# Optimization experiments

Measured on AMD Instinct MI355X. Metric: run time of the kernel, lower is better.

## Reference

```python
import jax, jax.numpy as jnp
import numpy as np

NODE_DIM = 128
EDGE_DIM = 16
HIDDEN = 128
B = 2
N = 20000
M = 320000


def setup_inputs() -> dict:
    key = jax.random.key(0)
    ks = jax.random.split(key, 20)

    def w(k, shape):
        return (jax.random.normal(k, shape, jnp.float32) / jnp.sqrt(shape[0])).astype(jnp.float32)

    X = jax.random.normal(ks[0], (B, N, NODE_DIM), jnp.float32)
    E = jax.random.normal(ks[1], (B, M, EDGE_DIM), jnp.float32)
    edges = jax.random.randint(ks[2], (B, M, 2), 0, N)
    return {
        "X": X, "E": E, "edges": edges,
        # node_mlp: Linear(node_dim,hidden) -> ReLU -> Linear(hidden,hidden)
        "nW1": w(ks[3], (NODE_DIM, HIDDEN)), "nb1": jnp.zeros((HIDDEN,), jnp.float32),
        "nW2": w(ks[4], (HIDDEN, HIDDEN)), "nb2": jnp.zeros((HIDDEN,), jnp.float32),
        # edge_mlp: Linear(2*node_dim+edge_dim,hidden) -> ReLU -> Linear(hidden,hidden)
        "eW1": w(ks[5], (2 * NODE_DIM + EDGE_DIM, HIDDEN)), "eb1": jnp.zeros((HIDDEN,), jnp.float32),
        "eW2": w(ks[6], (HIDDEN, HIDDEN)), "eb2": jnp.zeros((HIDDEN,), jnp.float32),
        # edge_proj: Linear(edge_dim, hidden)
        "pW": w(ks[7], (EDGE_DIM, HIDDEN)), "pb": jnp.zeros((HIDDEN,), jnp.float32),
        # read: Linear(2*hidden,64) -> ReLU -> Linear(64,2)
        "rW1": w(ks[8], (2 * HIDDEN, 64)), "rb1": jnp.zeros((64,), jnp.float32),
        "rW2": w(ks[9], (64, 2)), "rb2": jnp.zeros((2,), jnp.float32),
        "gate_scale": jnp.float32(2.0),
    }


def _forward_one(X, E, edges, nW1, nb1, nW2, nb2, eW1, eb1, eW2, eb2,
                 pW, pb, rW1, rb1, rW2, rb2, gate_scale):
    n_nodes = X.shape[0]
    n_edges = E.shape[0]
    # Hx = relu(node_mlp(X))  (node_mlp already ends without activation)
    Hx = jax.nn.relu(jax.nn.relu(X @ nW1 + nb1) @ nW2 + nb2)  # [N, H]
    # gate from 3rd edge-feature column (edge_dim >= 3)
    gate = jnp.clip(1.0 + gate_scale * E[:, 2:3], 0.0, 3.0)  # [M, 1]
    src = edges[:, 0]
    dst = edges[:, 1]
    # per-edge message: concat(X[i], X[j], E[k]) -> MLP -> relu -> * gate
    eij = jnp.concatenate([X[src], X[dst], E], axis=-1)  # [M, 2*node_dim+edge_dim]
    m = jax.nn.relu(jax.nn.relu(eij @ eW1 + eb1) @ eW2 + eb2) * gate  # [M, H]
    # scatter-add to both endpoints (sum order irrelevant)
    agg = (jax.ops.segment_sum(m, src, num_segments=n_nodes)
           + jax.ops.segment_sum(m, dst, num_segments=n_nodes))  # [N, H]
    # edge context: mean of gated edge projections
    edge_ctx = jnp.sum(gate * (E @ pW + pb), axis=0) / (n_edges + 1e-6)  # [H]
    H = Hx + agg
    feat = jnp.concatenate([H.mean(axis=0), edge_ctx], axis=0)  # [2H]
    return jax.nn.relu(feat @ rW1 + rb1) @ rW2 + rb2  # [2]


def reference(X, E, edges, nW1, nb1, nW2, nb2, eW1, eb1, eW2, eb2,
              pW, pb, rW1, rb1, rW2, rb2, gate_scale):
    fn = jax.vmap(_forward_one, in_axes=(0, 0, 0) + (None,) * 15)
    return fn(X, E, edges, nW1, nb1, nW2, nb2, eW1, eb1, eW2, eb2,
              pW, pb, rW1, rb1, rW2, rb2, gate_scale)  # [B, 2]
```

## Files before the change

### kernel.cpp

```cpp
#include <hip/hip_runtime.h>

typedef short bf16x8 __attribute__((ext_vector_type(8)));
typedef float f32x4 __attribute__((ext_vector_type(4)));

#define NB 2
#define NN 20000
#define ME 320000
#define STRIPES 64

__device__ __forceinline__ unsigned short f2bf(float f) {
  union { float f; unsigned int u; } v; v.f = f;
  unsigned int r = (v.u + 0x7FFFu + ((v.u >> 16) & 1u)) >> 16;
  return (unsigned short)r;
}

__device__ __forceinline__ f32x4 mfma16(bf16x8 a, bf16x8 b, f32x4 c) {
  return __builtin_amdgcn_mfma_f32_16x16x32_bf16(a, b, c, 0, 0, 0);
}


__global__ void cvt_x_kernel(const float* __restrict__ X, short* __restrict__ Xbf) {
  int i = blockIdx.x * 256 + threadIdx.x;
  const float4* p = reinterpret_cast<const float4*>(X) + (size_t)i * 2;
  float4 a = p[0], b = p[1];
  bf16x8 v;
  v[0]=(short)f2bf(a.x); v[1]=(short)f2bf(a.y); v[2]=(short)f2bf(a.z); v[3]=(short)f2bf(a.w);
  v[4]=(short)f2bf(b.x); v[5]=(short)f2bf(b.y); v[6]=(short)f2bf(b.z); v[7]=(short)f2bf(b.w);
  reinterpret_cast<bf16x8*>(Xbf)[i] = v;
}

__global__ void prep_w_kernel(const float* __restrict__ eW1, const float* __restrict__ eW2,
                              const float* __restrict__ nW1, const float* __restrict__ nW2,
                              const float* __restrict__ pW,
                              short* __restrict__ ew1T, short* __restrict__ ew2T,
                              short* __restrict__ nw1T, short* __restrict__ nw2T,
                              short* __restrict__ pwT) {
  int c = blockIdx.x;
  int t = threadIdx.x;
  for (int k = t; k < 288; k += 256)
    ew1T[c * 288 + k] = (k < 272) ? (short)f2bf(eW1[(size_t)k * 128 + c]) : (short)0;
  if (t < 128) {
    ew2T[c * 128 + t] = (short)f2bf(eW2[(size_t)t * 128 + c]);
    nw1T[c * 128 + t] = (short)f2bf(nW1[(size_t)t * 128 + c]);
    nw2T[c * 128 + t] = (short)f2bf(nW2[(size_t)t * 128 + c]);
  }
  if (t < 32) pwT[c * 32 + t] = (t < 16) ? (short)f2bf(pW[(size_t)t * 128 + c]) : (short)0;
}


template<bool XBF>
__global__ __launch_bounds__(256, 2) void edge_kernel(
    const short* __restrict__ Xbf, const float* __restrict__ X,
    const float* __restrict__ E, const int* __restrict__ edges,
    const short* __restrict__ ew1T, const short* __restrict__ ew2T,
    const short* __restrict__ pwT, const float* __restrict__ eb1,
    const float* __restrict__ eb2, const float* __restrict__ gsp,
    float* __restrict__ edge_acc) {
  __shared__ __align__(16) short A_lds[64 * 296];
  __shared__ __align__(16) short h1_lds[64 * 136];
  __shared__ float gate_lds[64];

  const int tid = threadIdx.x;
  const int lane = tid & 63;
  const int w = tid >> 6;
  const int fc = lane & 15;
  const int fg = lane >> 4;
  const int ncol0 = w * 32;
  const int b = blockIdx.y;

  const float gs = gsp[0];
  const float* E_b = E + (size_t)b * ME * 16;
  const int* edges_b = edges + (size_t)b * ME * 2;
  const short* Xbf_b = Xbf + (size_t)b * NN * 128;
  const float* X_b = X + (size_t)b * NN * 128;

  bf16x8 B1[2][9], B2[2][4], PWf[2];
  float eb1v[2], eb2v[2];
#pragma unroll
  for (int nt = 0; nt < 2; ++nt) {
    int col = ncol0 + nt * 16 + fc;
#pragma unroll
    for (int kt = 0; kt < 9; ++kt)
      B1[nt][kt] = *reinterpret_cast<const bf16x8*>(ew1T + col * 288 + kt * 32 + fg * 8);
#pragma unroll
    for (int kt = 0; kt < 4; ++kt)
      B2[nt][kt] = *reinterpret_cast<const bf16x8*>(ew2T + col * 128 + kt * 32 + fg * 8);
    PWf[nt] = *reinterpret_cast<const bf16x8*>(pwT + col * 32 + fg * 8);
    eb1v[nt] = eb1[col];
    eb2v[nt] = eb2[col];
  }

  float accm0 = 0.f, accm1 = 0.f, accp0 = 0.f, accp1 = 0.f, accg = 0.f;

  for (int it = 0; it < 4; ++it) {
    const int t = blockIdx.x * 4 + it;
    const int e0 = t * 64;
    if (XBF) {
#pragma unroll
      for (int p = 0; p < 8; ++p) {
        int row = p * 16 + (tid >> 4);
        int chunk = tid & 15;
        int e = row & 63, half = row >> 6;
        int node = edges_b[(size_t)(e0 + e) * 2 + half];
        uint4 v = reinterpret_cast<const uint4*>(Xbf_b + (size_t)node * 128)[chunk];
        *reinterpret_cast<uint4*>(&A_lds[e * 296 + half * 128 + chunk * 8]) = v;
      }
    } else {
#pragma unroll
      for (int p = 0; p < 16; ++p) {
        int slot = p * 256 + tid;
        int row = slot >> 5, chunk = slot & 31;
        int e = row & 63, half = row >> 6;
        int node = edges_b[(size_t)(e0 + e) * 2 + half];
        float4 f = reinterpret_cast<const float4*>(X_b + (size_t)node * 128)[chunk];
        ushort4 v; v.x = f2bf(f.x); v.y = f2bf(f.y); v.z = f2bf(f.z); v.w = f2bf(f.w);
        *reinterpret_cast<ushort4*>(&A_lds[e * 296 + half * 128 + chunk * 4]) = v;
      }
    }
    if (tid < 128) {
      int e = tid >> 1, half = tid & 1;
      const float4* pe = reinterpret_cast<const float4*>(E_b + (size_t)(e0 + e) * 16 + half * 8);
      float4 f0 = pe[0], f1 = pe[1];
      bf16x8 v;
      v[0]=(short)f2bf(f0.x); v[1]=(short)f2bf(f0.y); v[2]=(short)f2bf(f0.z); v[3]=(short)f2bf(f0.w);
      v[4]=(short)f2bf(f1.x); v[5]=(short)f2bf(f1.y); v[6]=(short)f2bf(f1.z); v[7]=(short)f2bf(f1.w);
      *reinterpret_cast<bf16x8*>(&A_lds[e * 296 + 256 + half * 8]) = v;
    } else {
      int e2 = (tid - 128) >> 1, half2 = (tid - 128) & 1;
      bf16x8 z = {0, 0, 0, 0, 0, 0, 0, 0};
      *reinterpret_cast<bf16x8*>(&A_lds[e2 * 296 + 272 + half2 * 8]) = z;
    }
    if (tid < 64) {
      float e2v = E_b[(size_t)(e0 + tid) * 16 + 2];
      gate_lds[tid] = fminf(fmaxf(1.f + gs * e2v, 0.f), 3.f);
    }
    __syncthreads();
    if (w == 0) accg += gate_lds[lane];

    f32x4 zf = {0.f, 0.f, 0.f, 0.f};
#pragma unroll
    for (int rt = 0; rt < 4; ++rt) {
      const short* arow = &A_lds[(rt * 16 + fc) * 296 + fg * 8];
      f32x4 a0 = zf, a1 = zf;
#pragma unroll
      for (int kt = 0; kt < 9; ++kt) {
        bf16x8 av = *reinterpret_cast<const bf16x8*>(arow + kt * 32);
        a0 = mfma16(av, B1[0][kt], a0);
        a1 = mfma16(av, B1[1][kt], a1);
      }
      bf16x8 av8 = *reinterpret_cast<const bf16x8*>(arow + 256);
      f32x4 p0 = mfma16(av8, PWf[0], zf);
      f32x4 p1 = mfma16(av8, PWf[1], zf);
#pragma unroll
      for (int r = 0; r < 4; ++r) {
        int row = rt * 16 + fg * 4 + r;
        float g = gate_lds[row];
        accp0 += p0[r] * g;
        accp1 += p1[r] * g;
        h1_lds[row * 136 + ncol0 + fc] = (short)f2bf(fmaxf(a0[r] + eb1v[0], 0.f));
        h1_lds[row * 136 + ncol0 + 16 + fc] = (short)f2bf(fmaxf(a1[r] + eb1v[1], 0.f));
      }
    }
    __syncthreads();
#pragma unroll
    for (int rt = 0; rt < 4; ++rt) {
      const short* hrow = &h1_lds[(rt * 16 + fc) * 136 + fg * 8];
      f32x4 a0 = zf, a1 = zf;
#pragma unroll
      for (int kt = 0; kt < 4; ++kt) {
        bf16x8 hv = *reinterpret_cast<const bf16x8*>(hrow + kt * 32);
        a0 = mfma16(hv, B2[0][kt], a0);
        a1 = mfma16(hv, B2[1][kt], a1);
      }
#pragma unroll
      for (int r = 0; r < 4; ++r) {
        int row = rt * 16 + fg * 4 + r;
        float g = gate_lds[row];
        accm0 += fmaxf(a0[r] + eb2v[0], 0.f) * g;
        accm1 += fmaxf(a1[r] + eb2v[1], 0.f) * g;
      }
    }
    __syncthreads();
  }

  accm0 += __shfl_xor(accm0, 16); accm0 += __shfl_xor(accm0, 32);
  accm1 += __shfl_xor(accm1, 16); accm1 += __shfl_xor(accm1, 32);
  accp0 += __shfl_xor(accp0, 16); accp0 += __shfl_xor(accp0, 32);
  accp1 += __shfl_xor(accp1, 16); accp1 += __shfl_xor(accp1, 32);
  const int stripe = blockIdx.x & (STRIPES - 1);
  float* base = edge_acc + ((size_t)b * STRIPES + stripe) * 264;
  if (fg == 0) {
    atomicAdd(base + ncol0 + fc, accm0);
    atomicAdd(base + ncol0 + 16 + fc, accm1);
    atomicAdd(base + 128 + ncol0 + fc, accp0);
    atomicAdd(base + 128 + ncol0 + 16 + fc, accp1);
  }
  if (w == 0) {
#pragma unroll
    for (int off = 1; off < 64; off <<= 1) accg += __shfl_xor(accg, off);
    if (lane == 0) atomicAdd(base + 256, accg);
  }
}


template<bool XBF>
__global__ __launch_bounds__(256, 2) void node_kernel(
    const short* __restrict__ Xbf, const float* __restrict__ X,
    const short* __restrict__ nw1T, const short* __restrict__ nw2T,
    const float* __restrict__ nb1, const float* __restrict__ nb2,
    float* __restrict__ node_acc) {
  __shared__ __align__(16) short A_lds[64 * 136];
  __shared__ __align__(16) short h1_lds[64 * 136];
  const int tid = threadIdx.x;
  const int lane = tid & 63;
  const int w = tid >> 6;
  const int fc = lane & 15;
  const int fg = lane >> 4;
  const int ncol0 = w * 32;
  const int b = blockIdx.y;
  const short* Xbf_b = Xbf + (size_t)b * NN * 128;
  const float* X_b = X + (size_t)b * NN * 128;

  bf16x8 B1[2][4], B2[2][4];
  float b1v[2], b2v[2];
#pragma unroll
  for (int nt = 0; nt < 2; ++nt) {
    int col = ncol0 + nt * 16 + fc;
#pragma unroll
    for (int kt = 0; kt < 4; ++kt) {
      B1[nt][kt] = *reinterpret_cast<const bf16x8*>(nw1T + col * 128 + kt * 32 + fg * 8);
      B2[nt][kt] = *reinterpret_cast<const bf16x8*>(nw2T + col * 128 + kt * 32 + fg * 8);
    }
    b1v[nt] = nb1[col];
    b2v[nt] = nb2[col];
  }
  float acc0 = 0.f, acc1 = 0.f;
  for (int t = blockIdx.x; t < 313; t += 157) {
    const int n0 = t * 64;
    if (XBF) {
#pragma unroll
      for (int p = 0; p < 4; ++p) {
        int row = p * 16 + (tid >> 4);
        int chunk = tid & 15;
        int node = n0 + row;
        uint4 v = {0, 0, 0, 0};
        if (node < NN) v = reinterpret_cast<const uint4*>(Xbf_b + (size_t)node * 128)[chunk];
        *reinterpret_cast<uint4*>(&A_lds[row * 136 + chunk * 8]) = v;
      }
    } else {
#pragma unroll
      for (int p = 0; p < 8; ++p) {
        int slot = p * 256 + tid;
        int row = slot >> 5, chunk = slot & 31;
        int node = n0 + row;
        ushort4 v = {0, 0, 0, 0};
        if (node < NN) {
          float4 f = reinterpret_cast<const float4*>(X_b + (size_t)node * 128)[chunk];
          v.x = f2bf(f.x); v.y = f2bf(f.y); v.z = f2bf(f.z); v.w = f2bf(f.w);
        }
        *reinterpret_cast<ushort4*>(&A_lds[row * 136 + chunk * 4]) = v;
      }
    }
    __syncthreads();
    f32x4 zf = {0.f, 0.f, 0.f, 0.f};
#pragma unroll
    for (int rt = 0; rt < 4; ++rt) {
      const short* arow = &A_lds[(rt * 16 + fc) * 136 + fg * 8];
      f32x4 a0 = zf, a1 = zf;
#pragma unroll
      for (int kt = 0; kt < 4; ++kt) {
        bf16x8 av = *reinterpret_cast<const bf16x8*>(arow + kt * 32);
        a0 = mfma16(av, B1[0][kt], a0);
        a1 = mfma16(av, B1[1][kt], a1);
      }
#pragma unroll
      for (int r = 0; r < 4; ++r) {
        int row = rt * 16 + fg * 4 + r;
        h1_lds[row * 136 + ncol0 + fc] = (short)f2bf(fmaxf(a0[r] + b1v[0], 0.f));
        h1_lds[row * 136 + ncol0 + 16 + fc] = (short)f2bf(fmaxf(a1[r] + b1v[1], 0.f));
      }
    }
    __syncthreads();
#pragma unroll
    for (int rt = 0; rt < 4; ++rt) {
      const short* hrow = &h1_lds[(rt * 16 + fc) * 136 + fg * 8];
      f32x4 a0 = zf, a1 = zf;
#pragma unroll
      for (int kt = 0; kt < 4; ++kt) {
        bf16x8 hv = *reinterpret_cast<const bf16x8*>(hrow + kt * 32);
        a0 = mfma16(hv, B2[0][kt], a0);
        a1 = mfma16(hv, B2[1][kt], a1);
      }
#pragma unroll
      for (int r = 0; r < 4; ++r) {
        int row = n0 + rt * 16 + fg * 4 + r;
        if (row < NN) {
          acc0 += fmaxf(a0[r] + b2v[0], 0.f);
          acc1 += fmaxf(a1[r] + b2v[1], 0.f);
        }
      }
    }
    __syncthreads();
  }
  acc0 += __shfl_xor(acc0, 16); acc0 += __shfl_xor(acc0, 32);
  acc1 += __shfl_xor(acc1, 16); acc1 += __shfl_xor(acc1, 32);
  if (fg == 0) {
    const int stripe = blockIdx.x & (STRIPES - 1);
    float* base = node_acc + ((size_t)b * STRIPES + stripe) * 128;
    atomicAdd(base + ncol0 + fc, acc0);
    atomicAdd(base + ncol0 + 16 + fc, acc1);
  }
}


__global__ void final_kernel(const float* __restrict__ edge_acc, const float* __restrict__ node_acc,
                             const float* __restrict__ pb, const float* __restrict__ rW1,
                             const float* __restrict__ rb1, const float* __restrict__ rW2,
                             const float* __restrict__ rb2, float* __restrict__ out) {
  int b = blockIdx.x;
  int j = threadIdx.x;
  __shared__ float feat[256];
  __shared__ float h[64];
  const float* ea = edge_acc + (size_t)b * STRIPES * 264;
  const float* na = node_acc + (size_t)b * STRIPES * 128;
  float ms = 0.f, ps = 0.f, hs = 0.f, gsum = 0.f;
  for (int s = 0; s < STRIPES; ++s) {
    ms += ea[s * 264 + j];
    ps += ea[s * 264 + 128 + j];
    hs += na[s * 128 + j];
    gsum += ea[s * 264 + 256];
  }
  feat[j] = (hs + 2.f * ms) * (1.f / (float)NN);
  feat[128 + j] = (ps + gsum * pb[j]) / ((float)ME + 1e-6f);
  __syncthreads();
  if (j < 64) {
    float a = rb1[j];
    for (int i = 0; i < 256; ++i) a += feat[i] * rW1[i * 64 + j];
    h[j] = fmaxf(a, 0.f);
  }
  __syncthreads();
  if (j < 2) {
    float a = rb2[j];
    for (int i = 0; i < 64; ++i) a += h[i] * rW2[i * 2 + j];
    out[b * 2 + j] = a;
  }
}


extern "C" void kernel_launch(void* const* d_in, const int* in_sizes, int n_in,
                              void* d_out, int out_size, void* d_ws, size_t ws_size,
                              hipStream_t stream) {
  const float* X = (const float*)d_in[0];
  const float* E = (const float*)d_in[1];
  const int* edges = (const int*)d_in[2];
  const float* nW1 = (const float*)d_in[3];
  const float* nb1 = (const float*)d_in[4];
  const float* nW2 = (const float*)d_in[5];
  const float* nb2 = (const float*)d_in[6];
  const float* eW1 = (const float*)d_in[7];
  const float* eb1 = (const float*)d_in[8];
  const float* eW2 = (const float*)d_in[9];
  const float* eb2 = (const float*)d_in[10];
  const float* pW = (const float*)d_in[11];
  const float* pb = (const float*)d_in[12];
  const float* rW1 = (const float*)d_in[13];
  const float* rb1 = (const float*)d_in[14];
  const float* rW2 = (const float*)d_in[15];
  const float* rb2 = (const float*)d_in[16];
  const float* gscale = (const float*)d_in[17];
  float* out = (float*)d_out;

  char* ws = (char*)d_ws;
  size_t off = 0;
  auto alloc = [&](size_t sz) -> void* {
    void* p = ws + off;
    off = (off + sz + 255) & ~(size_t)255;
    return p;
  };
  short* ew1T = (short*)alloc(288 * 128 * 2);
  short* ew2T = (short*)alloc(128 * 128 * 2);
  short* nw1T = (short*)alloc(128 * 128 * 2);
  short* nw2T = (short*)alloc(128 * 128 * 2);
  short* pwT  = (short*)alloc(32 * 128 * 2);
  size_t acc_floats = (size_t)NB * STRIPES * 264 + (size_t)NB * STRIPES * 128;
  float* acc = (float*)alloc(acc_floats * 4);
  float* edge_acc = acc;
  float* node_acc = acc + (size_t)NB * STRIPES * 264;
  size_t xbf_bytes = (size_t)NB * NN * 128 * 2;
  size_t off_before_xbf = off;
  short* Xbf = (short*)alloc(xbf_bytes);
  bool use_xbf = (off_before_xbf + xbf_bytes) <= ws_size;

  hipMemsetAsync(acc, 0, acc_floats * 4, stream);
  prep_w_kernel<<<dim3(128), dim3(256), 0, stream>>>(eW1, eW2, nW1, nW2, pW,
                                                     ew1T, ew2T, nw1T, nw2T, pwT);
  if (use_xbf) {
    cvt_x_kernel<<<dim3(2500), dim3(256), 0, stream>>>(X, Xbf);
    edge_kernel<true><<<dim3(1250, 2), dim3(256), 0, stream>>>(
        Xbf, X, E, edges, ew1T, ew2T, pwT, eb1, eb2, gscale, edge_acc);
    node_kernel<true><<<dim3(157, 2), dim3(256), 0, stream>>>(
        Xbf, X, nw1T, nw2T, nb1, nb2, node_acc);
  } else {
    edge_kernel<false><<<dim3(1250, 2), dim3(256), 0, stream>>>(
        Xbf, X, E, edges, ew1T, ew2T, pwT, eb1, eb2, gscale, edge_acc);
    node_kernel<false><<<dim3(157, 2), dim3(256), 0, stream>>>(
        Xbf, X, nw1T, nw2T, nb1, nb2, node_acc);
  }
  final_kernel<<<dim3(NB), dim3(128), 0, stream>>>(edge_acc, node_acc, pb, rW1, rb1, rW2, rb2, out);
}
```

Measured before the change: 242.1 us.

## Fuse X bf16 conversion into node kernel and software-pipeline edge gathers

Removes the separate X-to-bf16 conversion kernel: the node MLP kernel now converts X and writes the bf16 copy as it loads each tile, and runs first. The edge kernel becomes software-pipelined, with a double-buffered index and gate area, prefetching the next tile's gathered rows and edge features into registers while the current tile's MFMAs run. Each edge block now handles 8 tiles instead of 4, so fewer blocks reload the weight fragments. The cost is higher register pressure from holding prefetched data, which may hurt occupancy.

```diff
diff --git a/kernel.cpp b/kernel.cpp
--- a/kernel.cpp
+++ b/kernel.cpp
@@ -7,6 +7,7 @@
 #define NN 20000
 #define ME 320000
 #define STRIPES 64
+#define NT 8
 
 __device__ __forceinline__ unsigned short f2bf(float f) {
   union { float f; unsigned int u; } v; v.f = f;
@@ -14,19 +15,15 @@
   return (unsigned short)r;
 }
 
-__device__ __forceinline__ f32x4 mfma16(bf16x8 a, bf16x8 b, f32x4 c) {
-  return __builtin_amdgcn_mfma_f32_16x16x32_bf16(a, b, c, 0, 0, 0);
-}
-
-
-__global__ void cvt_x_kernel(const float* __restrict__ X, short* __restrict__ Xbf) {
-  int i = blockIdx.x * 256 + threadIdx.x;
-  const float4* p = reinterpret_cast<const float4*>(X) + (size_t)i * 2;
-  float4 a = p[0], b = p[1];
+__device__ __forceinline__ bf16x8 pack2(float4 a, float4 b) {
   bf16x8 v;
   v[0]=(short)f2bf(a.x); v[1]=(short)f2bf(a.y); v[2]=(short)f2bf(a.z); v[3]=(short)f2bf(a.w);
   v[4]=(short)f2bf(b.x); v[5]=(short)f2bf(b.y); v[6]=(short)f2bf(b.z); v[7]=(short)f2bf(b.w);
-  reinterpret_cast<bf16x8*>(Xbf)[i] = v;
+  return v;
+}
+
+__device__ __forceinline__ f32x4 mfma16(bf16x8 a, bf16x8 b, f32x4 c) {
+  return __builtin_amdgcn_mfma_f32_16x16x32_bf16(a, b, c, 0, 0, 0);
 }
 
 __global__ void prep_w_kernel(const float* __restrict__ eW1, const float* __restrict__ eW2,
@@ -48,164 +45,9 @@
 }
 
 
-template<bool XBF>
-__global__ __launch_bounds__(256, 2) void edge_kernel(
-    const short* __restrict__ Xbf, const float* __restrict__ X,
-    const float* __restrict__ E, const int* __restrict__ edges,
-    const short* __restrict__ ew1T, const short* __restrict__ ew2T,
-    const short* __restrict__ pwT, const float* __restrict__ eb1,
-    const float* __restrict__ eb2, const float* __restrict__ gsp,
-    float* __restrict__ edge_acc) {
-  __shared__ __align__(16) short A_lds[64 * 296];
-  __shared__ __align__(16) short h1_lds[64 * 136];
-  __shared__ float gate_lds[64];
-
-  const int tid = threadIdx.x;
-  const int lane = tid & 63;
-  const int w = tid >> 6;
-  const int fc = lane & 15;
-  const int fg = lane >> 4;
-  const int ncol0 = w * 32;
-  const int b = blockIdx.y;
-
-  const float gs = gsp[0];
-  const float* E_b = E + (size_t)b * ME * 16;
-  const int* edges_b = edges + (size_t)b * ME * 2;
-  const short* Xbf_b = Xbf + (size_t)b * NN * 128;
-  const float* X_b = X + (size_t)b * NN * 128;
-
-  bf16x8 B1[2][9], B2[2][4], PWf[2];
-  float eb1v[2], eb2v[2];
-#pragma unroll
-  for (int nt = 0; nt < 2; ++nt) {
-    int col = ncol0 + nt * 16 + fc;
-#pragma unroll
-    for (int kt = 0; kt < 9; ++kt)
-      B1[nt][kt] = *reinterpret_cast<const bf16x8*>(ew1T + col * 288 + kt * 32 + fg * 8);
-#pragma unroll
-    for (int kt = 0; kt < 4; ++kt)
-      B2[nt][kt] = *reinterpret_cast<const bf16x8*>(ew2T + col * 128 + kt * 32 + fg * 8);
-    PWf[nt] = *reinterpret_cast<const bf16x8*>(pwT + col * 32 + fg * 8);
-    eb1v[nt] = eb1[col];
-    eb2v[nt] = eb2[col];
-  }
-
-  float accm0 = 0.f, accm1 = 0.f, accp0 = 0.f, accp1 = 0.f, accg = 0.f;
-
-  for (int it = 0; it < 4; ++it) {
-    const int t = blockIdx.x * 4 + it;
-    const int e0 = t * 64;
-    if (XBF) {
-#pragma unroll
-      for (int p = 0; p < 8; ++p) {
-        int row = p * 16 + (tid >> 4);
-        int chunk = tid & 15;
-        int e = row & 63, half = row >> 6;
-        int node = edges_b[(size_t)(e0 + e) * 2 + half];
-        uint4 v = reinterpret_cast<const uint4*>(Xbf_b + (size_t)node * 128)[chunk];
-        *reinterpret_cast<uint4*>(&A_lds[e * 296 + half * 128 + chunk * 8]) = v;
-      }
-    } else {
-#pragma unroll
-      for (int p = 0; p < 16; ++p) {
-        int slot = p * 256 + tid;
-        int row = slot >> 5, chunk = slot & 31;
-        int e = row & 63, half = row >> 6;
-        int node = edges_b[(size_t)(e0 + e) * 2 + half];
-        float4 f = reinterpret_cast<const float4*>(X_b + (size_t)node * 128)[chunk];
-        ushort4 v; v.x = f2bf(f.x); v.y = f2bf(f.y); v.z = f2bf(f.z); v.w = f2bf(f.w);
-        *reinterpret_cast<ushort4*>(&A_lds[e * 296 + half * 128 + chunk * 4]) = v;
-      }
-    }
-    if (tid < 128) {
-      int e = tid >> 1, half = tid & 1;
-      const float4* pe = reinterpret_cast<const float4*>(E_b + (size_t)(e0 + e) * 16 + half * 8);
-      float4 f0 = pe[0], f1 = pe[1];
-      bf16x8 v;
-      v[0]=(short)f2bf(f0.x); v[1]=(short)f2bf(f0.y); v[2]=(short)f2bf(f0.z); v[3]=(short)f2bf(f0.w);
-      v[4]=(short)f2bf(f1.x); v[5]=(short)f2bf(f1.y); v[6]=(short)f2bf(f1.z); v[7]=(short)f2bf(f1.w);
-      *reinterpret_cast<bf16x8*>(&A_lds[e * 296 + 256 + half * 8]) = v;
-    } else {
-      int e2 = (tid - 128) >> 1, half2 = (tid - 128) & 1;
-      bf16x8 z = {0, 0, 0, 0, 0, 0, 0, 0};
-      *reinterpret_cast<bf16x8*>(&A_lds[e2 * 296 + 272 + half2 * 8]) = z;
-    }
-    if (tid < 64) {
-      float e2v = E_b[(size_t)(e0 + tid) * 16 + 2];
-      gate_lds[tid] = fminf(fmaxf(1.f + gs * e2v, 0.f), 3.f);
-    }
-    __syncthreads();
-    if (w == 0) accg += gate_lds[lane];
-
-    f32x4 zf = {0.f, 0.f, 0.f, 0.f};
-#pragma unroll
-    for (int rt = 0; rt < 4; ++rt) {
-      const short* arow = &A_lds[(rt * 16 + fc) * 296 + fg * 8];
-      f32x4 a0 = zf, a1 = zf;
-#pragma unroll
-      for (int kt = 0; kt < 9; ++kt) {
-        bf16x8 av = *reinterpret_cast<const bf16x8*>(arow + kt * 32);
-        a0 = mfma16(av, B1[0][kt], a0);
-        a1 = mfma16(av, B1[1][kt], a1);
-      }
-      bf16x8 av8 = *reinterpret_cast<const bf16x8*>(arow + 256);
-      f32x4 p0 = mfma16(av8, PWf[0], zf);
-      f32x4 p1 = mfma16(av8, PWf[1], zf);
-#pragma unroll
-      for (int r = 0; r < 4; ++r) {
-        int row = rt * 16 + fg * 4 + r;
-        float g = gate_lds[row];
-        accp0 += p0[r] * g;
-        accp1 += p1[r] * g;
-        h1_lds[row * 136 + ncol0 + fc] = (short)f2bf(fmaxf(a0[r] + eb1v[0], 0.f));
-        h1_lds[row * 136 + ncol0 + 16 + fc] = (short)f2bf(fmaxf(a1[r] + eb1v[1], 0.f));
-      }
-    }
-    __syncthreads();
-#pragma unroll
-    for (int rt = 0; rt < 4; ++rt) {
-      const short* hrow = &h1_lds[(rt * 16 + fc) * 136 + fg * 8];
-      f32x4 a0 = zf, a1 = zf;
-#pragma unroll
-      for (int kt = 0; kt < 4; ++kt) {
-        bf16x8 hv = *reinterpret_cast<const bf16x8*>(hrow + kt * 32);
-        a0 = mfma16(hv, B2[0][kt], a0);
-        a1 = mfma16(hv, B2[1][kt], a1);
-      }
-#pragma unroll
-      for (int r = 0; r < 4; ++r) {
-        int row = rt * 16 + fg * 4 + r;
-        float g = gate_lds[row];
-        accm0 += fmaxf(a0[r] + eb2v[0], 0.f) * g;
-        accm1 += fmaxf(a1[r] + eb2v[1], 0.f) * g;
-      }
-    }
-    __syncthreads();
-  }
-
-  accm0 += __shfl_xor(accm0, 16); accm0 += __shfl_xor(accm0, 32);
-  accm1 += __shfl_xor(accm1, 16); accm1 += __shfl_xor(accm1, 32);
-  accp0 += __shfl_xor(accp0, 16); accp0 += __shfl_xor(accp0, 32);
-  accp1 += __shfl_xor(accp1, 16); accp1 += __shfl_xor(accp1, 32);
-  const int stripe = blockIdx.x & (STRIPES - 1);
-  float* base = edge_acc + ((size_t)b * STRIPES + stripe) * 264;
-  if (fg == 0) {
-    atomicAdd(base + ncol0 + fc, accm0);
-    atomicAdd(base + ncol0 + 16 + fc, accm1);
-    atomicAdd(base + 128 + ncol0 + fc, accp0);
-    atomicAdd(base + 128 + ncol0 + 16 + fc, accp1);
-  }
-  if (w == 0) {
-#pragma unroll
-    for (int off = 1; off < 64; off <<= 1) accg += __shfl_xor(accg, off);
-    if (lane == 0) atomicAdd(base + 256, accg);
-  }
-}
-
-
-template<bool XBF>
+template<bool WRITEBF>
 __global__ __launch_bounds__(256, 2) void node_kernel(
-    const short* __restrict__ Xbf, const float* __restrict__ X,
+    const float* __restrict__ X, short* __restrict__ Xbf,
     const short* __restrict__ nw1T, const short* __restrict__ nw2T,
     const float* __restrict__ nb1, const float* __restrict__ nb2,
     float* __restrict__ node_acc) {
@@ -218,8 +60,8 @@
   const int fg = lane >> 4;
   const int ncol0 = w * 32;
   const int b = blockIdx.y;
-  const short* Xbf_b = Xbf + (size_t)b * NN * 128;
   const float* X_b = X + (size_t)b * NN * 128;
+  short* Xbf_b = Xbf + (size_t)b * NN * 128;
 
   bf16x8 B1[2][4], B2[2][4];
   float b1v[2], b2v[2];
@@ -234,73 +76,61 @@
     b1v[nt] = nb1[col];
     b2v[nt] = nb2[col];
   }
+
+  const int n0 = blockIdx.x * 64;
+#pragma unroll
+  for (int p = 0; p < 8; ++p) {
+    int slot = p * 256 + tid;
+    int row = slot >> 5, chunk = slot & 31;
+    int node = n0 + row;
+    ushort4 v = {0, 0, 0, 0};
+    if (node < NN) {
+      float4 f = *reinterpret_cast<const float4*>(X_b + (size_t)node * 128 + chunk * 4);
+      v.x = f2bf(f.x); v.y = f2bf(f.y); v.z = f2bf(f.z); v.w = f2bf(f.w);
+      if (WRITEBF) *reinterpret_cast<ushort4*>(Xbf_b + (size_t)node * 128 + chunk * 4) = v;
+    }
+    *reinterpret_cast<ushort4*>(&A_lds[row * 136 + chunk * 4]) = v;
+  }
+  __syncthreads();
+
+  f32x4 zf = {0.f, 0.f, 0.f, 0.f};
   float acc0 = 0.f, acc1 = 0.f;
-  for (int t = blockIdx.x; t < 313; t += 157) {
-    const int n0 = t * 64;
-    if (XBF) {
-#pragma unroll
-      for (int p = 0; p < 4; ++p) {
-        int row = p * 16 + (tid >> 4);
-        int chunk = tid & 15;
-        int node = n0 + row;
-        uint4 v = {0, 0, 0, 0};
-        if (node < NN) v = reinterpret_cast<const uint4*>(Xbf_b + (size_t)node * 128)[chunk];
-        *reinterpret_cast<uint4*>(&A_lds[row * 136 + chunk * 8]) = v;
+#pragma unroll
+  for (int rt = 0; rt < 4; ++rt) {
+    const short* arow = &A_lds[(rt * 16 + fc) * 136 + fg * 8];
+    f32x4 a0 = zf, a1 = zf;
+#pragma unroll
+    for (int kt = 0; kt < 4; ++kt) {
+      bf16x8 av = *reinterpret_cast<const bf16x8*>(arow + kt * 32);
+      a0 = mfma16(av, B1[0][kt], a0);
+      a1 = mfma16(av, B1[1][kt], a1);
+    }
+#pragma unroll
+    for (int r = 0; r < 4; ++r) {
+      int row = rt * 16 + fg * 4 + r;
+      h1_lds[row * 136 + ncol0 + fc] = (short)f2bf(fmaxf(a0[r] + b1v[0], 0.f));
+      h1_lds[row * 136 + ncol0 + 16 + fc] = (short)f2bf(fmaxf(a1[r] + b1v[1], 0.f));
+    }
+  }
+  __syncthreads();
+#pragma unroll
+  for (int rt = 0; rt < 4; ++rt) {
+    const short* hrow = &h1_lds[(rt * 16 + fc) * 136 + fg * 8];
+    f32x4 a0 = zf, a1 = zf;
+#pragma unroll
+    for (int kt = 0; kt < 4; ++kt) {
+      bf16x8 hv = *reinterpret_cast<const bf16x8*>(hrow + kt * 32);
+      a0 = mfma16(hv, B2[0][kt], a0);
+      a1 = mfma16(hv, B2[1][kt], a1);
+    }
+#pragma unroll
+    for (int r = 0; r < 4; ++r) {
+      int row = n0 + rt * 16 + fg * 4 + r;
+      if (row < NN) {
+        acc0 += fmaxf(a0[r] + b2v[0], 0.f);
+        acc1 += fmaxf(a1[r] + b2v[1], 0.f);
       }
-    } else {
-#pragma unroll
-      for (int p = 0; p < 8; ++p) {
-        int slot = p * 256 + tid;
-        int row = slot >> 5, chunk = slot & 31;
-        int node = n0 + row;
-        ushort4 v = {0, 0, 0, 0};
-        if (node < NN) {
-          float4 f = reinterpret_cast<const float4*>(X_b + (size_t)node * 128)[chunk];
-          v.x = f2bf(f.x); v.y = f2bf(f.y); v.z = f2bf(f.z); v.w = f2bf(f.w);
-        }
-        *reinterpret_cast<ushort4*>(&A_lds[row * 136 + chunk * 4]) = v;
-      }
-    }
-    __syncthreads();
-    f32x4 zf = {0.f, 0.f, 0.f, 0.f};
-#pragma unroll
-    for (int rt = 0; rt < 4; ++rt) {
-      const short* arow = &A_lds[(rt * 16 + fc) * 136 + fg * 8];
-      f32x4 a0 = zf, a1 = zf;
-#pragma unroll
-      for (int kt = 0; kt < 4; ++kt) {
-        bf16x8 av = *reinterpret_cast<const bf16x8*>(arow + kt * 32);
-        a0 = mfma16(av, B1[0][kt], a0);
-        a1 = mfma16(av, B1[1][kt], a1);
-      }
-#pragma unroll
-      for (int r = 0; r < 4; ++r) {
-        int row = rt * 16 + fg * 4 + r;
-        h1_lds[row * 136 + ncol0 + fc] = (short)f2bf(fmaxf(a0[r] + b1v[0], 0.f));
-        h1_lds[row * 136 + ncol0 + 16 + fc] = (short)f2bf(fmaxf(a1[r] + b1v[1], 0.f));
-      }
-    }
-    __syncthreads();
-#pragma unroll
-    for (int rt = 0; rt < 4; ++rt) {
-      const short* hrow = &h1_lds[(rt * 16 + fc) * 136 + fg * 8];
-      f32x4 a0 = zf, a1 = zf;
-#pragma unroll
-      for (int kt = 0; kt < 4; ++kt) {
-        bf16x8 hv = *reinterpret_cast<const bf16x8*>(hrow + kt * 32);
-        a0 = mfma16(hv, B2[0][kt], a0);
-        a1 = mfma16(hv, B2[1][kt], a1);
-      }
-#pragma unroll
-      for (int r = 0; r < 4; ++r) {
-        int row = n0 + rt * 16 + fg * 4 + r;
-        if (row < NN) {
-          acc0 += fmaxf(a0[r] + b2v[0], 0.f);
-          acc1 += fmaxf(a1[r] + b2v[1], 0.f);
-        }
-      }
-    }
-    __syncthreads();
+    }
   }
   acc0 += __shfl_xor(acc0, 16); acc0 += __shfl_xor(acc0, 32);
   acc1 += __shfl_xor(acc1, 16); acc1 += __shfl_xor(acc1, 32);
@@ -310,6 +140,190 @@
     atomicAdd(base + ncol0 + fc, acc0);
     atomicAdd(base + ncol0 + 16 + fc, acc1);
   }
+}
+
+
+template<bool XBF>
+__global__ __launch_bounds__(256, 2) void edge_kernel(
+    const short* __restrict__ Xbf, const float* __restrict__ X,
+    const float* __restrict__ E, const int* __restrict__ edges,
+    const short* __restrict__ ew1T, const short* __restrict__ ew2T,
+    const short* __restrict__ pwT, const float* __restrict__ eb1,
+    const float* __restrict__ eb2, const float* __restrict__ gsp,
+    float* __restrict__ edge_acc) {
+  __shared__ __align__(16) short A_lds[64 * 296];
+  __shared__ __align__(16) short h1_lds[64 * 136];
+  __shared__ float gate_lds[2][64];
+  __shared__ int idx_lds[2][128];
+
+  const int tid = threadIdx.x;
+  const int lane = tid & 63;
+  const int w = tid >> 6;
+  const int fc = lane & 15;
+  const int fg = lane >> 4;
+  const int ncol0 = w * 32;
+  const int b = blockIdx.y;
+
+  const float gs = gsp[0];
+  const float* E_b = E + (size_t)b * ME * 16;
+  const int* edges_b = edges + (size_t)b * ME * 2;
+  const short* Xbf_b = Xbf + (size_t)b * NN * 128;
+  const float* X_b = X + (size_t)b * NN * 128;
+  const int tile0 = blockIdx.x * NT;
+
+  bf16x8 B1[2][9], B2[2][4], PWf[2];
+  float eb1v[2], eb2v[2];
+#pragma unroll
+  for (int nt = 0; nt < 2; ++nt) {
+    int col = ncol0 + nt * 16 + fc;
+#pragma unroll
+    for (int kt = 0; kt < 9; ++kt)
+      B1[nt][kt] = *reinterpret_cast<const bf16x8*>(ew1T + col * 288 + kt * 32 + fg * 8);
+#pragma unroll
+    for (int kt = 0; kt < 4; ++kt)
+      B2[nt][kt] = *reinterpret_cast<const bf16x8*>(ew2T + col * 128 + kt * 32 + fg * 8);
+    PWf[nt] = *reinterpret_cast<const bf16x8*>(pwT + col * 32 + fg * 8);
+    eb1v[nt] = eb1[col];
+    eb2v[nt] = eb2[col];
+  }
+
+  const int grow = tid >> 1;
+  const int ge = grow & 63;
+  const int gsd = grow >> 6;
+  const int gpos = (ge << 1) | gsd;
+  const int ghalf = tid & 1;
+  const int et = tid >> 2, q = tid & 3;
+
+#define GATHER8(node, v0, v1, v2, v3, v4, v5, v6, v7)                                   \
+  if (XBF) {                                                                            \
+    const bf16x8* gp = reinterpret_cast<const bf16x8*>(Xbf_b + (size_t)(node)*128 + ghalf*64); \
+    v0 = gp[0]; v1 = gp[1]; v2 = gp[2]; v3 = gp[3];                                     \
+    v4 = gp[4]; v5 = gp[5]; v6 = gp[6]; v7 = gp[7];                                     \
+  } else {                                                                              \
+    const float4* gp = reinterpret_cast<const float4*>(X_b + (size_t)(node)*128 + ghalf*64); \
+    v0 = pack2(gp[0], gp[1]);  v1 = pack2(gp[2], gp[3]);                                \
+    v2 = pack2(gp[4], gp[5]);  v3 = pack2(gp[6], gp[7]);                                \
+    v4 = pack2(gp[8], gp[9]);  v5 = pack2(gp[10], gp[11]);                              \
+    v6 = pack2(gp[12], gp[13]); v7 = pack2(gp[14], gp[15]);                             \
+  }
+
+#define STORE8(v0, v1, v2, v3, v4, v5, v6, v7)                                          \
+  {                                                                                     \
+    bf16x8* aw8 = reinterpret_cast<bf16x8*>(&A_lds[ge * 296 + gsd * 128 + ghalf * 64]); \
+    aw8[0] = v0; aw8[1] = v1; aw8[2] = v2; aw8[3] = v3;                                 \
+    aw8[4] = v4; aw8[5] = v5; aw8[6] = v6; aw8[7] = v7;                                 \
+  }
+
+  if (tid < 64) {
+    bf16x8 z = {0, 0, 0, 0, 0, 0, 0, 0};
+    *reinterpret_cast<bf16x8*>(&A_lds[tid * 296 + 272]) = z;
+    *reinterpret_cast<bf16x8*>(&A_lds[tid * 296 + 280]) = z;
+  }
+  {
+    const int e0 = tile0 * 64;
+    int node = edges_b[(size_t)e0 * 2 + gpos];
+    bf16x8 s0, s1, s2, s3, s4, s5, s6, s7;
+    GATHER8(node, s0, s1, s2, s3, s4, s5, s6, s7);
+    STORE8(s0, s1, s2, s3, s4, s5, s6, s7);
+    float4 ev = *reinterpret_cast<const float4*>(E_b + (size_t)e0 * 16 + tid * 4);
+    ushort4 evb; evb.x = f2bf(ev.x); evb.y = f2bf(ev.y); evb.z = f2bf(ev.z); evb.w = f2bf(ev.w);
+    *reinterpret_cast<ushort4*>(&A_lds[et * 296 + 256 + q * 4]) = evb;
+    if (q == 0) gate_lds[0][et] = fminf(fmaxf(1.f + gs * ev.z, 0.f), 3.f);
+    if (tid < 128) idx_lds[1][tid] = edges_b[(size_t)(tile0 + 1) * 64 * 2 + tid];
+  }
+  __syncthreads();
+
+  float accm0 = 0.f, accm1 = 0.f, accp0 = 0.f, accp1 = 0.f, accg = 0.f;
+  const f32x4 zf = {0.f, 0.f, 0.f, 0.f};
+
+  for (int it = 0; it < NT; ++it) {
+    const int cur = it & 1, nxt = (it + 1) & 1;
+    const bool hasn1 = (it + 1 < NT);
+    const bool hasn2 = (it + 2 < NT);
+    const int e0n = (hasn1 ? (tile0 + it + 1) : tile0) * 64;
+    const int e0n2 = (hasn2 ? (tile0 + it + 2) : tile0) * 64;
+
+    float4 epre = *reinterpret_cast<const float4*>(E_b + (size_t)e0n * 16 + tid * 4);
+    int idxpre = 0;
+    if (tid < 128) idxpre = edges_b[(size_t)e0n2 * 2 + tid];
+    const int node = idx_lds[nxt][gpos];
+    bf16x8 p0v, p1v, p2v, p3v, p4v, p5v, p6v, p7v;
+    GATHER8(node, p0v, p1v, p2v, p3v, p4v, p5v, p6v, p7v);
+
+#pragma unroll
+    for (int rt = 0; rt < 4; ++rt) {
+      const short* arow = &A_lds[(rt * 16 + fc) * 296 + fg * 8];
+      f32x4 a0 = zf, a1 = zf;
+#pragma unroll
+      for (int kt = 0; kt < 9; ++kt) {
+        bf16x8 av = *reinterpret_cast<const bf16x8*>(arow + kt * 32);
+        a0 = mfma16(av, B1[0][kt], a0);
+        a1 = mfma16(av, B1[1][kt], a1);
+      }
+      bf16x8 av8 = *reinterpret_cast<const bf16x8*>(arow + 256);
+      f32x4 q0 = mfma16(av8, PWf[0], zf);
+      f32x4 q1 = mfma16(av8, PWf[1], zf);
+#pragma unroll
+      for (int r = 0; r < 4; ++r) {
+        int row = rt * 16 + fg * 4 + r;
+        float g = gate_lds[cur][row];
+        accp0 += q0[r] * g;
+        accp1 += q1[r] * g;
+        h1_lds[row * 136 + ncol0 + fc] = (short)f2bf(fmaxf(a0[r] + eb1v[0], 0.f));
+        h1_lds[row * 136 + ncol0 + 16 + fc] = (short)f2bf(fmaxf(a1[r] + eb1v[1], 0.f));
+      }
+    }
+    __syncthreads();
+
+    if (hasn1) {
+      STORE8(p0v, p1v, p2v, p3v, p4v, p5v, p6v, p7v);
+      ushort4 evb; evb.x = f2bf(epre.x); evb.y = f2bf(epre.y); evb.z = f2bf(epre.z); evb.w = f2bf(epre.w);
+      *reinterpret_cast<ushort4*>(&A_lds[et * 296 + 256 + q * 4]) = evb;
+      if (q == 0) gate_lds[nxt][et] = fminf(fmaxf(1.f + gs * epre.z, 0.f), 3.f);
+      if (tid < 128) idx_lds[cur][tid] = idxpre;
+    }
+
+    if (w == 0) accg += gate_lds[cur][lane];
+#pragma unroll
+    for (int rt = 0; rt < 4; ++rt) {
+      const short* hrow = &h1_lds[(rt * 16 + fc) * 136 + fg * 8];
+      f32x4 a0 = zf, a1 = zf;
+#pragma unroll
+      for (int kt = 0; kt < 4; ++kt) {
+        bf16x8 hv = *reinterpret_cast<const bf16x8*>(hrow + kt * 32);
+        a0 = mfma16(hv, B2[0][kt], a0);
+        a1 = mfma16(hv, B2[1][kt], a1);
+      }
+#pragma unroll
+      for (int r = 0; r < 4; ++r) {
+        int row = rt * 16 + fg * 4 + r;
+        float g = gate_lds[cur][row];
+        accm0 += fmaxf(a0[r] + eb2v[0], 0.f) * g;
+        accm1 += fmaxf(a1[r] + eb2v[1], 0.f) * g;
+      }
+    }
+    __syncthreads();
+  }
+
+  accm0 += __shfl_xor(accm0, 16); accm0 += __shfl_xor(accm0, 32);
+  accm1 += __shfl_xor(accm1, 16); accm1 += __shfl_xor(accm1, 32);
+  accp0 += __shfl_xor(accp0, 16); accp0 += __shfl_xor(accp0, 32);
+  accp1 += __shfl_xor(accp1, 16); accp1 += __shfl_xor(accp1, 32);
+  const int stripe = blockIdx.x & (STRIPES - 1);
+  float* base = edge_acc + ((size_t)b * STRIPES + stripe) * 264;
+  if (fg == 0) {
+    atomicAdd(base + ncol0 + fc, accm0);
+    atomicAdd(base + ncol0 + 16 + fc, accm1);
+    atomicAdd(base + 128 + ncol0 + fc, accp0);
+    atomicAdd(base + 128 + ncol0 + 16 + fc, accp1);
+  }
+  if (w == 0) {
+#pragma unroll
+    for (int off = 1; off < 64; off <<= 1) accg += __shfl_xor(accg, off);
+    if (lane == 0) atomicAdd(base + 256, accg);
+  }
+#undef GATHER8
+#undef STORE8
 }
 
 
@@ -395,16 +409,13 @@
   prep_w_kernel<<<dim3(128), dim3(256), 0, stream>>>(eW1, eW2, nW1, nW2, pW,
                                                      ew1T, ew2T, nw1T, nw2T, pwT);
   if (use_xbf) {
-    cvt_x_kernel<<<dim3(2500), dim3(256), 0, stream>>>(X, Xbf);
-    edge_kernel<true><<<dim3(1250, 2), dim3(256), 0, stream>>>(
+    node_kernel<true><<<dim3(313, 2), dim3(256), 0, stream>>>(X, Xbf, nw1T, nw2T, nb1, nb2, node_acc);
+    edge_kernel<true><<<dim3(625, 2), dim3(256), 0, stream>>>(
         Xbf, X, E, edges, ew1T, ew2T, pwT, eb1, eb2, gscale, edge_acc);
-    node_kernel<true><<<dim3(157, 2), dim3(256), 0, stream>>>(
-        Xbf, X, nw1T, nw2T, nb1, nb2, node_acc);
   } else {
-    edge_kernel<false><<<dim3(1250, 2), dim3(256), 0, stream>>>(
+    node_kernel<false><<<dim3(313, 2), dim3(256), 0, stream>>>(X, Xbf, nw1T, nw2T, nb1, nb2, node_acc);
+    edge_kernel<false><<<dim3(625, 2), dim3(256), 0, stream>>>(
         Xbf, X, E, edges, ew1T, ew2T, pwT, eb1, eb2, gscale, edge_acc);
-    node_kernel<false><<<dim3(157, 2), dim3(256), 0, stream>>>(
-        Xbf, X, nw1T, nw2T, nb1, nb2, node_acc);
   }
   final_kernel<<<dim3(NB), dim3(128), 0, stream>>>(edge_acc, node_acc, pb, rW1, rb1, rW2, rb2, out);
 }
```

Result: faster. 235.4 us (-2.8%).
